# Performance work log

Hardware: AMD Instinct MI355X
Metric: run time of the kernel (lower is better)

The kernel has to match this reference:

```python
import jax, jax.numpy as jnp
import numpy as np

B, T, DIM = 8, 1024, 2048
H, NKV, HD = 16, 4, 128
G = H // NKV          # query heads per kv head
BASE = 10000.0
EPS = 1e-6
SCALE = HD ** -0.5


def _rope_tables(seqlen):
    inv = 1.0 / (BASE ** (np.arange(0, HD, 2, dtype=np.float32) / HD))  # [HD/2]
    t = np.arange(seqlen, dtype=np.float32)
    f = np.outer(t, inv)  # [T, HD/2]
    return jnp.asarray(np.cos(f)), jnp.asarray(np.sin(f))


def _rms_norm(x):
    return x * jax.lax.rsqrt(jnp.mean(x * x, axis=-1, keepdims=True) + EPS)


def _rope(x, cos, sin):
    # x: [B, heads, T, HD]; cos/sin broadcast over batch and heads
    x1, x2 = x[..., : HD // 2], x[..., HD // 2 :]
    return jnp.concatenate([x1 * cos - x2 * sin, x2 * cos + x1 * sin], axis=-1)


def setup_inputs() -> dict:
    key = jax.random.key(0)
    ks = jax.random.split(key, 6)
    s = 1.0 / np.sqrt(DIM)
    return {
        "x": jax.random.normal(ks[0], (B, T, DIM), dtype=jnp.float32),
        "Wq": jax.random.normal(ks[1], (DIM, DIM), dtype=jnp.float32) * s,
        "Wk": jax.random.normal(ks[2], (NKV * HD, DIM), dtype=jnp.float32) * s,
        "Wv": jax.random.normal(ks[3], (NKV * HD, DIM), dtype=jnp.float32) * s,
        "Wproj": jax.random.normal(ks[4], (DIM, DIM), dtype=jnp.float32) * s,
        "q_gain": jnp.ones((H,), dtype=jnp.float32),
    }


def reference(x, Wq, Wk, Wv, Wproj, q_gain):
    bsz, seqlen, dim = x.shape
    # projections -> [B, heads, T, HD]
    q = (x @ Wq.T).reshape(bsz, seqlen, H, HD).transpose(0, 2, 1, 3)
    k = (x @ Wk.T).reshape(bsz, seqlen, NKV, HD).transpose(0, 2, 1, 3)
    v = (x @ Wv.T).reshape(bsz, seqlen, NKV, HD).transpose(0, 2, 1, 3)

    cos, sin = _rope_tables(seqlen)
    cos, sin = cos[None, None], sin[None, None]
    q = _rope(_rms_norm(q), cos, sin) * q_gain[None, :, None, None]
    k = _rope(_rms_norm(k), cos, sin)

    # GQA: group query heads instead of materializing repeated k/v
    qg = q.reshape(bsz, NKV, G, seqlen, HD)
    scores = jnp.einsum("bngtd,bnsd->bngts", qg, k) * SCALE  # [B,NKV,G,T,T]
    causal = jnp.tril(jnp.ones((seqlen, seqlen), dtype=bool))
    scores = jnp.where(causal, scores, jnp.finfo(scores.dtype).min)
    p = jax.nn.softmax(scores, axis=-1)
    y = jnp.einsum("bngts,bnsd->bngtd", p, v)  # [B,NKV,G,T,HD]
    y = y.transpose(0, 3, 1, 2, 4).reshape(bsz, seqlen, dim)

    # XSA: subtract self-value projection per kv head
    y_g = y.reshape(bsz, seqlen, NKV, G, HD)
    v_t = v.transpose(0, 2, 1, 3)  # [B,T,NKV,HD]
    vn = v_t / (jnp.linalg.norm(v_t, axis=-1, keepdims=True) + 1e-8)
    vn = vn[:, :, :, None, :]  # broadcast over group dim
    proj_comp = jnp.sum(y_g * vn, axis=-1, keepdims=True) * vn
    y = (y_g - proj_comp).reshape(bsz, seqlen, dim)

    return y @ Wproj.T
```

## Files before the change

kernel.cpp:

```cpp
#include <hip/hip_runtime.h>
#include <stdint.h>

#define T_SEQ 1024

typedef _Float16 f16x8 __attribute__((ext_vector_type(8)));
typedef float f32x4 __attribute__((ext_vector_type(4)));

typedef __attribute__((address_space(1))) const uint8_t* gptr_t;
typedef __attribute__((address_space(3))) uint8_t* lptr_t;

__device__ __forceinline__ void gload16(const _Float16* g, _Float16* l) {
  __builtin_amdgcn_global_load_lds((gptr_t)g, (lptr_t)l, 16, 0, 0);
}

__global__ __launch_bounds__(256) void convert_all(
    const float* __restrict__ x, const float* __restrict__ Wq,
    const float* __restrict__ Wk, const float* __restrict__ Wv,
    const float* __restrict__ Wp, _Float16* __restrict__ xh,
    _Float16* __restrict__ wqh, _Float16* __restrict__ wkh,
    _Float16* __restrict__ wvh, _Float16* __restrict__ wph) {
  int i = blockIdx.x * 256 + threadIdx.x;
  const float* in;
  _Float16* out;
  int base;
  if (i < 2097152)      { in = x;  out = xh;  base = 0; }
  else if (i < 2621440) { in = Wq; out = wqh; base = 2097152; }
  else if (i < 2752512) { in = Wk; out = wkh; base = 2621440; }
  else if (i < 2883584) { in = Wv; out = wvh; base = 2752512; }
  else                  { in = Wp; out = wph; base = 2883584; }
  int j = i - base;
  const float4* p = (const float4*)in + (size_t)j * 2;
  float4 a = p[0], b = p[1];
  f16x8 o;
  o[0] = (_Float16)a.x; o[1] = (_Float16)a.y; o[2] = (_Float16)a.z; o[3] = (_Float16)a.w;
  o[4] = (_Float16)b.x; o[5] = (_Float16)b.y; o[6] = (_Float16)b.z; o[7] = (_Float16)b.w;
  ((f16x8*)out)[j] = o;
}

template <typename OutT>
__global__ __launch_bounds__(512, 2) void gemm256(
    const _Float16* __restrict__ A, const _Float16* __restrict__ B,
    OutT* __restrict__ C0, int ldc0, int nb0,
    OutT* __restrict__ C1, int ldc1, int nbn) {
  __shared__ _Float16 As[2][256][64];
  __shared__ _Float16 Bs[2][256][64];
  const int tid = threadIdx.x;
  const int wave = tid >> 6, lane = tid & 63;
  const int lm = lane & 15, lq = lane >> 4;
  const int wm = wave >> 2, wn = wave & 3;

  const int qx = (int)gridDim.x >> 3;
  const int swz = ((int)blockIdx.x & 7) * qx + ((int)blockIdx.x >> 3);
  const int bm = swz / nbn, bn = swz % nbn;

  const int r8 = lane >> 3;
  const int csw = ((lane & 7) ^ r8) * 8;
  const _Float16* Asrc = A + (size_t)(bm * 256 + wave * 16 + r8) * 2048 + csw;
  const _Float16* Bsrc = B + (size_t)(bn * 256 + wave * 16 + r8) * 2048 + csw;

  f32x4 acc[8][4];
#pragma unroll
  for (int m = 0; m < 8; m++)
#pragma unroll
    for (int n = 0; n < 4; n++) acc[m][n] = (f32x4){0.f, 0.f, 0.f, 0.f};

  f16x8 af[4][2], bf[4][2];

  auto stageA = [&](int t, int h) {
    const _Float16* s = Asrc + (size_t)h * 128 * 2048 + t * 64;
    _Float16* d = &As[t & 1][h * 128 + wave * 16][0];
    gload16(s, d);
    gload16(s + (size_t)8 * 2048, d + 8 * 64);
  };
  auto stageB = [&](int t, int h) {
    const _Float16* s = Bsrc + (size_t)h * 128 * 2048 + t * 64;
    _Float16* d = &Bs[t & 1][h * 128 + wave * 16][0];
    gload16(s, d);
    gload16(s + (size_t)8 * 2048, d + 8 * 64);
  };
  auto lda = [&](int b, int mh) {
#pragma unroll
    for (int m = 0; m < 4; m++)
#pragma unroll
      for (int ks = 0; ks < 2; ks++)
        af[m][ks] = *(const f16x8*)&As[b][wm * 128 + mh * 64 + m * 16 + lm]
                                      [(((ks * 4 + lq)) ^ (lm & 7)) * 8];
  };
  auto ldb = [&](int b, int nh) {
#pragma unroll
    for (int n = 0; n < 2; n++)
#pragma unroll
      for (int ks = 0; ks < 2; ks++)
        bf[nh * 2 + n][ks] = *(const f16x8*)&Bs[b][wn * 64 + nh * 32 + n * 16 + lm]
                                               [(((ks * 4 + lq)) ^ (lm & 7)) * 8];
  };
  auto mfmaQ = [&](int mh, int nh) {
    __builtin_amdgcn_s_setprio(1);
#pragma unroll
    for (int m = 0; m < 4; m++)
#pragma unroll
      for (int n = 0; n < 2; n++)
#pragma unroll
        for (int ks = 0; ks < 2; ks++)
          acc[mh * 4 + m][nh * 2 + n] = __builtin_amdgcn_mfma_f32_16x16x32_f16(
              af[m][ks], bf[nh * 2 + n][ks], acc[mh * 4 + m][nh * 2 + n], 0, 0, 0);
    __builtin_amdgcn_s_setprio(0);
  };

#define BAR() __builtin_amdgcn_s_barrier()
#define LGKM0() asm volatile("s_waitcnt lgkmcnt(0)" ::: "memory")

  stageA(0, 0); stageA(0, 1);
  stageB(0, 0); stageB(0, 1);
  stageB(1, 0); stageB(1, 1);
  asm volatile("s_waitcnt vmcnt(4)" ::: "memory");
  BAR();

  const int NT = 32;
  for (int j = 0; j < NT / 2; ++j) {
    const int t1 = 2 * j + 1, t2 = 2 * j + 2, t3 = 2 * j + 3;
    const bool s2 = t2 < NT, s3 = t3 < NT;
    lda(0, 0); ldb(0, 0); stageA(t1, 0);
    BAR(); LGKM0(); mfmaQ(0, 0); BAR();
    ldb(0, 1); stageA(t1, 1);
    BAR(); LGKM0(); mfmaQ(0, 1); BAR();
    lda(0, 1); if (s2) stageB(t2, 0);
    BAR(); LGKM0(); mfmaQ(1, 0); BAR();
    if (s2) stageB(t2, 1);
    BAR(); mfmaQ(1, 1);
    if (s2) { asm volatile("s_waitcnt vmcnt(4)" ::: "memory"); }
    else    { asm volatile("s_waitcnt vmcnt(0)" ::: "memory"); }
    BAR();
    lda(1, 0); ldb(1, 0); if (s2) stageA(t2, 0);
    BAR(); LGKM0(); mfmaQ(0, 0); BAR();
    ldb(1, 1); if (s2) stageA(t2, 1);
    BAR(); LGKM0(); mfmaQ(0, 1); BAR();
    lda(1, 1); if (s3) stageB(t3, 0);
    BAR(); LGKM0(); mfmaQ(1, 0); BAR();
    if (s3) stageB(t3, 1);
    BAR(); mfmaQ(1, 1);
    asm volatile("s_waitcnt vmcnt(4)" ::: "memory");
    BAR();
  }
#undef BAR
#undef LGKM0

  OutT* C;
  int ldc, cb;
  if (bn < nb0) { C = C0; ldc = ldc0; cb = bn * 256; }
  else          { C = C1; ldc = ldc1; cb = (bn - nb0) * 256; }
#pragma unroll
  for (int m = 0; m < 8; m++) {
    size_t gr = (size_t)(bm * 256 + wm * 128 + m * 16 + lq * 4);
#pragma unroll
    for (int n = 0; n < 4; n++) {
      int gc = cb + wn * 64 + n * 16 + lm;
#pragma unroll
      for (int r = 0; r < 4; r++)
        C[(gr + r) * ldc + gc] = (OutT)acc[m][n][r];
    }
  }
}

__global__ __launch_bounds__(256) void transpose16(const _Float16* __restrict__ in,
                                                   _Float16* __restrict__ out) {
  __shared__ _Float16 Ts[64][72];
  int tr = blockIdx.x * 64, tc = blockIdx.y * 64;
  int r0 = threadIdx.x >> 3, c8 = (threadIdx.x & 7) * 8;
#pragma unroll
  for (int i = 0; i < 2; i++) {
    int r = r0 + i * 32;
    *(f16x8*)&Ts[r][c8] = *(const f16x8*)&in[(size_t)(tr + r) * 1024 + tc + c8];
  }
  __syncthreads();
#pragma unroll
  for (int i = 0; i < 2; i++) {
    int oc = r0 + i * 32;
    f16x8 o;
#pragma unroll
    for (int j = 0; j < 8; j++) o[j] = Ts[c8 + j][oc];
    *(f16x8*)&out[(size_t)(tc + oc) * 8192 + tr + c8] = o;
  }
}

__global__ __launch_bounds__(256) void rmsrope_all(_Float16* __restrict__ qh,
                                                   _Float16* __restrict__ kvb,
                                                   const float* __restrict__ gain) {
  int gw = blockIdx.x * 4 + (threadIdx.x >> 6);
  int lane = threadIdx.x & 63;
  _Float16* row;
  int t;
  float g = 1.0f;
  if (gw < 131072) {
    int h = gw & 15;
    t = (gw >> 4) & 1023;
    row = qh + (size_t)gw * 128;
    g = gain[h] * 0.08838834764831845f * 1.4426950408889634f;
  } else {
    int gk = gw - 131072;
    t = (gk >> 2) & 1023;
    row = kvb + (size_t)(gk >> 2) * 1024 + (gk & 3) * 128;
  }
  float x1 = (float)row[lane], x2 = (float)row[lane + 64];
  float ss = x1 * x1 + x2 * x2;
#pragma unroll
  for (int m = 1; m < 64; m <<= 1) ss += __shfl_xor(ss, m);
  float scale = rsqrtf(ss * (1.0f / 128.0f) + 1e-6f) * g;
  float inv = exp2f((float)lane * -0.2076205059304601f);
  float ang = (float)t * inv;
  float c = cosf(ang), s = sinf(ang);
  row[lane]      = (_Float16)((x1 * c - x2 * s) * scale);
  row[lane + 64] = (_Float16)((x2 * c + x1 * s) * scale);
}

__global__ __launch_bounds__(256, 2) void attn_mfma(const _Float16* __restrict__ q,
                                                    const _Float16* __restrict__ k,
                                                    const _Float16* __restrict__ vT,
                                                    _Float16* __restrict__ y) {
  __shared__ _Float16 Ks[2][4][64][32];
  __shared__ _Float16 VTs[2][2][128][32];
  __shared__ _Float16 Ps[4][32][64];
  int h = blockIdx.y, b = blockIdx.z;
  int kvh = h >> 2;
  int tid = threadIdx.x, wave = tid >> 6, lane = tid & 63;
  int lm = lane & 15, lq = lane >> 4;
  int srow = lane >> 2, scol = (lane & 3) * 8;

  for (int pass = 0; pass < 2; ++pass) {
    int qt = pass ? (int)blockIdx.x : 7 - (int)blockIdx.x;

    f16x8 qf[2][4];
#pragma unroll
    for (int mt = 0; mt < 2; mt++) {
      const _Float16* qp =
          q + ((size_t)((b * T_SEQ + qt * 128 + wave * 32 + mt * 16 + lm) * 16 + h)) * 128 +
          lq * 8;
#pragma unroll
      for (int ks = 0; ks < 4; ks++) qf[mt][ks] = *(const f16x8*)(qp + ks * 32);
    }

    f32x4 O[2][8];
#pragma unroll
    for (int mt = 0; mt < 2; mt++)
#pragma unroll
      for (int i = 0; i < 8; i++) O[mt][i] = (f32x4){0.f, 0.f, 0.f, 0.f};
    float mrow[2][4], lrow[2][4];
#pragma unroll
    for (int mt = 0; mt < 2; mt++)
#pragma unroll
      for (int r = 0; r < 4; r++) { mrow[mt][r] = -1e30f; lrow[mt][r] = 0.f; }

    const _Float16* kg =
        k + (size_t)(b * T_SEQ + srow) * 1024 + kvh * 128 + wave * 32 + scol;
    const _Float16* vg =
        vT + (size_t)(kvh * 128 + (wave >> 1) * 64 + srow) * 8192 + b * T_SEQ +
        (wave & 1) * 32 + scol;

    int wrow = qt * 128 + wave * 32;
    int nit = (qt + 1) * 2;

#pragma unroll
    for (int i = 0; i < 4; i++) {
      gload16(kg + (size_t)i * 16 * 1024, &Ks[0][wave][i * 16][0]);
      gload16(vg + (size_t)i * 16 * 8192, &VTs[0][wave & 1][(wave >> 1) * 64 + i * 16][0]);
    }
    kg += (size_t)64 * 1024;
    vg += 64;
    asm volatile("s_waitcnt vmcnt(0)" ::: "memory");
    __builtin_amdgcn_s_barrier();

    for (int it = 0; it < nit; ++it) {
      int cur = it & 1;
      int s0 = it * 64;
      if (it + 1 < nit) {
#pragma unroll
        for (int i = 0; i < 4; i++) {
          gload16(kg + (size_t)i * 16 * 1024, &Ks[cur ^ 1][wave][i * 16][0]);
          gload16(vg + (size_t)i * 16 * 8192,
                  &VTs[cur ^ 1][wave & 1][(wave >> 1) * 64 + i * 16][0]);
        }
        kg += (size_t)64 * 1024;
        vg += 64;
      }

      f32x4 S[2][4];
#pragma unroll
      for (int mt = 0; mt < 2; mt++)
#pragma unroll
        for (int ct = 0; ct < 4; ct++) S[mt][ct] = (f32x4){0.f, 0.f, 0.f, 0.f};
#pragma unroll
      for (int ct = 0; ct < 4; ct++)
#pragma unroll
        for (int ks = 0; ks < 4; ks++) {
          f16x8 bfr = *(const f16x8*)&Ks[cur][ks][ct * 16 + lm][lq * 8];
          S[0][ct] = __builtin_amdgcn_mfma_f32_16x16x32_f16(qf[0][ks], bfr, S[0][ct], 0, 0, 0);
          S[1][ct] = __builtin_amdgcn_mfma_f32_16x16x32_f16(qf[1][ks], bfr, S[1][ct], 0, 0, 0);
        }

      float p[2][4][4], al[2][4];
#pragma unroll
      for (int mt = 0; mt < 2; mt++) {
        bool need_mask = (s0 + 63 > wrow + mt * 16);
#pragma unroll
        for (int r = 0; r < 4; r++) {
          int grow = wrow + mt * 16 + lq * 4 + r;
          float mx = -1e30f;
#pragma unroll
          for (int ct = 0; ct < 4; ct++) {
            float sv = S[mt][ct][r];
            if (need_mask && (s0 + ct * 16 + lm > grow)) sv = -1e30f;
            p[mt][r][ct] = sv;
            mx = fmaxf(mx, sv);
          }
#pragma unroll
          for (int m = 1; m < 16; m <<= 1) mx = fmaxf(mx, __shfl_xor(mx, m));
          float mn = fmaxf(mrow[mt][r], mx);
          float a = exp2f(mrow[mt][r] - mn);
          mrow[mt][r] = mn;
          float rs = 0.f;
#pragma unroll
          for (int ct = 0; ct < 4; ct++) {
            float pv = exp2f(p[mt][r][ct] - mn);
            p[mt][r][ct] = pv;
            rs += pv;
          }
#pragma unroll
          for (int m = 1; m < 16; m <<= 1) rs += __shfl_xor(rs, m);
          lrow[mt][r] = lrow[mt][r] * a + rs;
          al[mt][r] = a;
        }
      }

#pragma unroll
      for (int mt = 0; mt < 2; mt++)
#pragma unroll
        for (int r = 0; r < 4; r++) {
          int prow = mt * 16 + lq * 4 + r;
#pragma unroll
          for (int ct = 0; ct < 4; ct++) {
            int cg = (ct * 2 + (lm >> 3)) ^ (prow & 7);
            Ps[wave][prow][cg * 8 + (lm & 7)] = (_Float16)p[mt][r][ct];
          }
        }
#pragma unroll
      for (int mt = 0; mt < 2; mt++)
#pragma unroll
        for (int ct = 0; ct < 8; ct++)
#pragma unroll
          for (int r = 0; r < 4; r++) O[mt][ct][r] *= al[mt][r];

#pragma unroll
      for (int ks2 = 0; ks2 < 2; ks2++) {
        f16x8 afr[2];
#pragma unroll
        for (int mt = 0; mt < 2; mt++) {
          int prow = mt * 16 + lm;
          int cg = (ks2 * 4 + lq) ^ (prow & 7);
          afr[mt] = *(const f16x8*)&Ps[wave][prow][cg * 8];
        }
#pragma unroll
        for (int ct = 0; ct < 8; ct++) {
          f16x8 bfr = *(const f16x8*)&VTs[cur][ks2][ct * 16 + lm][lq * 8];
          O[0][ct] = __builtin_amdgcn_mfma_f32_16x16x32_f16(afr[0], bfr, O[0][ct], 0, 0, 0);
          O[1][ct] = __builtin_amdgcn_mfma_f32_16x16x32_f16(afr[1], bfr, O[1][ct], 0, 0, 0);
        }
      }
      asm volatile("s_waitcnt vmcnt(0)" ::: "memory");
      __builtin_amdgcn_s_barrier();
    }

#pragma unroll
    for (int mt = 0; mt < 2; mt++) {
      float linv[4];
#pragma unroll
      for (int r = 0; r < 4; r++) linv[r] = 1.0f / lrow[mt][r];
      int qrow_base = wrow + mt * 16 + lq * 4;
#pragma unroll
      for (int ct = 0; ct < 8; ct++)
#pragma unroll
        for (int r = 0; r < 4; r++)
          y[((size_t)(b * T_SEQ + qrow_base + r) * 16 + h) * 128 + ct * 16 + lm] =
              (_Float16)(O[mt][ct][r] * linv[r]);
    }
  }
}

__global__ __launch_bounds__(256) void vreject(const _Float16* __restrict__ y,
                                               const _Float16* __restrict__ kvb,
                                               _Float16* __restrict__ yh) {
  int gw = blockIdx.x * 4 + (threadIdx.x >> 6);
  int lane = threadIdx.x & 63;
  int bt = gw >> 2, n = gw & 3;
  const _Float16* vrow = kvb + (size_t)bt * 1024 + 512 + n * 128;
  float v1 = (float)vrow[lane], v2 = (float)vrow[lane + 64];
  float ss = v1 * v1 + v2 * v2;
#pragma unroll
  for (int m = 1; m < 64; m <<= 1) ss += __shfl_xor(ss, m);
  float invn = 1.0f / (sqrtf(ss) + 1e-8f);
  float n1 = v1 * invn, n2 = v2 * invn;
  const _Float16* ybase = y + (size_t)bt * 2048 + n * 512;
  _Float16* obase = yh + (size_t)bt * 2048 + n * 512;
#pragma unroll
  for (int g = 0; g < 4; g++) {
    float y1 = (float)ybase[g * 128 + lane], y2 = (float)ybase[g * 128 + lane + 64];
    float d = y1 * n1 + y2 * n2;
#pragma unroll
    for (int m = 1; m < 64; m <<= 1) d += __shfl_xor(d, m);
    obase[g * 128 + lane]      = (_Float16)(y1 - d * n1);
    obase[g * 128 + lane + 64] = (_Float16)(y2 - d * n2);
  }
}

extern "C" void kernel_launch(void* const* d_in, const int* in_sizes, int n_in,
                              void* d_out, int out_size, void* d_ws, size_t ws_size,
                              hipStream_t stream) {
  const float* x    = (const float*)d_in[0];
  const float* Wq   = (const float*)d_in[1];
  const float* Wk   = (const float*)d_in[2];
  const float* Wv   = (const float*)d_in[3];
  const float* Wp   = (const float*)d_in[4];
  const float* gain = (const float*)d_in[5];
  float* out = (float*)d_out;

  char* w = (char*)d_ws;
  _Float16* xh   = (_Float16*)(w + 0);
  _Float16* wqh  = (_Float16*)(w + 32u * 1048576);
  _Float16* wkvh = (_Float16*)(w + 40u * 1048576);
  _Float16* wph  = (_Float16*)(w + 44u * 1048576);
  _Float16* qh   = (_Float16*)(w + 52u * 1048576);
  _Float16* kvb  = (_Float16*)(w + 84u * 1048576);
  _Float16* vTg  = (_Float16*)(w + 100u * 1048576);
  _Float16* ya   = (_Float16*)(w + 108u * 1048576);
  _Float16* yh2  = xh;

  convert_all<<<13312, 256, 0, stream>>>(x, Wq, Wk, Wv, Wp, xh, wqh,
                                         wkvh, wkvh + (size_t)512 * 2048, wph);

  gemm256<_Float16><<<384, 512, 0, stream>>>(xh, wqh, qh, 2048, 8, kvb, 1024, 12);

  transpose16<<<dim3(128, 8), 256, 0, stream>>>(kvb + 512, vTg);
  rmsrope_all<<<40960, 256, 0, stream>>>(qh, kvb, gain);

  attn_mfma<<<dim3(4, 16, 8), 256, 0, stream>>>(qh, kvb, vTg, ya);

  vreject<<<8192, 256, 0, stream>>>(ya, kvb, yh2);

  gemm256<float><<<256, 512, 0, stream>>>(yh2, wph, out, 2048, 8,
                                          (float*)nullptr, 2048, 8);
}
```

Measured before the change: 485.1 us.

## Add smaller-tile 128x256 GEMM with K=32 stages for QKV projection

Introduces a new GEMM kernel using 128x256 output tiles and 32-wide K stages with smaller LDS footprint, launched with 768 blocks instead of 384 for the fused QKV projection. The smaller tile and LDS usage allow higher occupancy (launch bounds 6 blocks) and better CU coverage on the 256-CU device. It trades lower data reuse per block and more barriers per K iteration (64 steps) for better load balance and latency hiding.

```diff
diff --git a/kernel.cpp b/kernel.cpp
--- a/kernel.cpp
+++ b/kernel.cpp
@@ -35,6 +35,87 @@
   o[0] = (_Float16)a.x; o[1] = (_Float16)a.y; o[2] = (_Float16)a.z; o[3] = (_Float16)a.w;
   o[4] = (_Float16)b.x; o[5] = (_Float16)b.y; o[6] = (_Float16)b.z; o[7] = (_Float16)b.w;
   ((f16x8*)out)[j] = o;
+}
+
+template <typename OutT>
+__global__ __launch_bounds__(512, 6) void gemm_h(
+    const _Float16* __restrict__ A, const _Float16* __restrict__ B,
+    OutT* __restrict__ C0, int ldc0, int nb0,
+    OutT* __restrict__ C1, int ldc1, int nbn) {
+  __shared__ _Float16 As[2][128][32];
+  __shared__ _Float16 Bs[2][256][32];
+  const int tid = threadIdx.x;
+  const int wave = tid >> 6, lane = tid & 63;
+  const int lm = lane & 15, lq = lane >> 4;
+  const int wm = wave >> 2, wn = wave & 3;
+
+  const int qx = (int)gridDim.x >> 3;
+  const int swz = ((int)blockIdx.x & 7) * qx + ((int)blockIdx.x >> 3);
+  const int bm = swz / nbn, bn = swz % nbn;
+
+  const int sr = tid >> 2;
+  const int scsw = ((tid & 3) ^ ((tid >> 3) & 3)) * 8;
+  const _Float16* Asrc = A + (size_t)(bm * 128 + sr) * 2048 + scsw;
+  const _Float16* Bsrc = B + (size_t)(bn * 256 + sr) * 2048 + scsw;
+
+  f32x4 acc[4][4];
+#pragma unroll
+  for (int m = 0; m < 4; m++)
+#pragma unroll
+    for (int n = 0; n < 4; n++) acc[m][n] = (f32x4){0.f, 0.f, 0.f, 0.f};
+
+  auto stage = [&](int t, int bi) {
+    gload16(Asrc + t * 32, &As[bi][wave * 16][0]);
+    gload16(Bsrc + t * 32, &Bs[bi][wave * 16][0]);
+    gload16(Bsrc + (size_t)128 * 2048 + t * 32, &Bs[bi][128 + wave * 16][0]);
+  };
+
+  const int lofs = (lq ^ ((lm >> 1) & 3)) * 8;
+
+  stage(0, 0);
+  asm volatile("s_waitcnt vmcnt(0)" ::: "memory");
+  __builtin_amdgcn_s_barrier();
+
+  const int NT = 64;
+  for (int t = 0; t < NT; ++t) {
+    const int cur = t & 1;
+    if (t + 1 < NT) stage(t + 1, cur ^ 1);
+
+    f16x8 af[4], bf[4];
+#pragma unroll
+    for (int m = 0; m < 4; m++)
+      af[m] = *(const f16x8*)&As[cur][wm * 64 + m * 16 + lm][lofs];
+#pragma unroll
+    for (int n = 0; n < 4; n++)
+      bf[n] = *(const f16x8*)&Bs[cur][wn * 64 + n * 16 + lm][lofs];
+
+    __builtin_amdgcn_s_setprio(1);
+#pragma unroll
+    for (int m = 0; m < 4; m++)
+#pragma unroll
+      for (int n = 0; n < 4; n++)
+        acc[m][n] = __builtin_amdgcn_mfma_f32_16x16x32_f16(af[m], bf[n], acc[m][n], 0, 0, 0);
+    __builtin_amdgcn_s_setprio(0);
+
+    asm volatile("s_waitcnt vmcnt(0)" ::: "memory");
+    __builtin_amdgcn_s_barrier();
+  }
+
+  OutT* C;
+  int ldc, cb;
+  if (bn < nb0) { C = C0; ldc = ldc0; cb = bn * 256; }
+  else          { C = C1; ldc = ldc1; cb = (bn - nb0) * 256; }
+#pragma unroll
+  for (int m = 0; m < 4; m++) {
+    size_t gr = (size_t)(bm * 128 + wm * 64 + m * 16 + lq * 4);
+#pragma unroll
+    for (int n = 0; n < 4; n++) {
+      int gc = cb + wn * 64 + n * 16 + lm;
+#pragma unroll
+      for (int r = 0; r < 4; r++)
+        C[(gr + r) * ldc + gc] = (OutT)acc[m][n][r];
+    }
+  }
 }
 
 template <typename OutT>
@@ -436,7 +517,7 @@
   convert_all<<<13312, 256, 0, stream>>>(x, Wq, Wk, Wv, Wp, xh, wqh,
                                          wkvh, wkvh + (size_t)512 * 2048, wph);
 
-  gemm256<_Float16><<<384, 512, 0, stream>>>(xh, wqh, qh, 2048, 8, kvb, 1024, 12);
+  gemm_h<_Float16><<<768, 512, 0, stream>>>(xh, wqh, qh, 2048, 8, kvb, 1024, 12);
 
   transpose16<<<dim3(128, 8), 256, 0, stream>>>(kvb + 512, vTg);
   rmsrope_all<<<40960, 256, 0, stream>>>(qh, kvb, gain);
```

Result: slower. 1.500 ms (+209.2%).
